# Kernel tuning notes

Measured on AMD Instinct MI355X. Metric: run time of the kernel, lower is better.

The kernel has to match this reference:

```python
import jax, jax.numpy as jnp
import numpy as np

B, T, D_IN = 64, 256, 256
H, N, W, R, D_OUT = 512, 128, 64, 4, 256
CTRL_IN = D_IN + R * W          # 512
IFACE = R * W + R + W + 1 + W + W + R * 3  # 465
EPS = 1e-8


def setup_inputs() -> dict:
    key = jax.random.key(0)
    ks = jax.random.split(key, 10)
    def lin(k, out_d, in_d):
        s = 1.0 / np.sqrt(in_d)
        return jax.random.uniform(k, (out_d, in_d), jnp.float32, -s, s)
    def vec(k, d, in_d):
        s = 1.0 / np.sqrt(in_d)
        return jax.random.uniform(k, (d,), jnp.float32, -s, s)
    return {
        'x': jax.random.normal(ks[0], (B, T, D_IN), jnp.float32),
        'W_ih': lin(ks[1], 4 * H, CTRL_IN),
        'W_hh': lin(ks[2], 4 * H, H),
        'b_ih': vec(ks[3], 4 * H, H),
        'b_hh': vec(ks[4], 4 * H, H),
        'W_int': lin(ks[5], IFACE, H),
        'b_int': vec(ks[6], IFACE, H),
        'W_out': lin(ks[7], D_OUT, H + R * W),
        'b_out': vec(ks[8], D_OUT, H + R * W),
    }


def _content_weights(mem, keys, strength):
    # mem: (b, n, w); keys: (b, r, w); strength: (b, r, 1) -> weights (b, r, n)
    dot = jnp.einsum('brw,bnw->brn', keys, mem)
    nm = jnp.maximum(jnp.linalg.norm(mem, axis=-1), EPS)      # (b, n)
    nk = jnp.maximum(jnp.linalg.norm(keys, axis=-1), EPS)     # (b, r)
    sim = dot / (nk[:, :, None] * nm[:, None, :])
    return jax.nn.softmax(strength * sim, axis=-1)


def reference(x, W_ih, W_hh, b_ih, b_hh, W_int, b_int, W_out, b_out):
    b = x.shape[0]

    def step(carry, x_t):
        h, c, mem, rv = carry
        ci = jnp.concatenate([x_t, rv.reshape(b, R * W)], axis=-1)
        gates = ci @ W_ih.T + b_ih + h @ W_hh.T + b_hh
        i_g, f_g, g_g, o_g = jnp.split(gates, 4, axis=-1)  # torch LSTM gate order
        c = jax.nn.sigmoid(f_g) * c + jax.nn.sigmoid(i_g) * jnp.tanh(g_g)
        h = jax.nn.sigmoid(o_g) * jnp.tanh(c)

        iface = h @ W_int.T + b_int
        idx = 0
        read_keys = iface[:, idx:idx + R * W].reshape(b, R, W); idx += R * W
        read_str = jax.nn.softplus(iface[:, idx:idx + R]) + 1.0; idx += R
        write_key = iface[:, idx:idx + W]; idx += W
        write_str = jax.nn.softplus(iface[:, idx:idx + 1]) + 1.0; idx += 1
        erase = jax.nn.sigmoid(iface[:, idx:idx + W]); idx += W
        write_vec = iface[:, idx:idx + W]; idx += W
        # read_modes are parsed in the original but never used -> skipped

        ww = _content_weights(mem, write_key[:, None, :], write_str[:, None, :])[:, 0, :]  # (b, n)
        mem = mem * (1.0 - ww[:, :, None] * erase[:, None, :]) + ww[:, :, None] * write_vec[:, None, :]

        rw = _content_weights(mem, read_keys, read_str[:, :, None])  # (b, r, n)
        rv = jnp.einsum('brn,bnw->brw', rw, mem)

        out = jnp.concatenate([h, rv.reshape(b, R * W)], axis=-1) @ W_out.T + b_out
        return (h, c, mem, rv), out

    init = (jnp.zeros((b, H), x.dtype), jnp.zeros((b, H), x.dtype),
            jnp.zeros((b, N, W), x.dtype), jnp.zeros((b, R, W), x.dtype))
    _, outs = jax.lax.scan(step, init, jnp.swapaxes(x, 0, 1))  # outs: (T, b, D_OUT)
    return outs[-1]  # return_sequence=False -> last timestep
```

## Files before the change

### kernel.cpp

```cpp
#include <hip/hip_runtime.h>
#include <math.h>

#define BB_   64
#define TT_   256
#define DIN_  256
#define HH_   512
#define NMEM_ 128
#define WWID_ 64
#define RR_   4
#define DOUT_ 256
#define CTRL_ 512
#define EPSV  1e-8f
#define NBLK  256
#define NTHR  512
#define OSTR  456
#define MPAD  65

__device__ __forceinline__ float sigm(float x){ return 1.f/(1.f+expf(-x)); }
__device__ __forceinline__ float softp(float x){ return (x>20.f)? x : log1pf(expf(x)); }
__device__ __forceinline__ float wredsum(float v){
  #pragma unroll
  for (int o=32;o>0;o>>=1) v += __shfl_xor(v,o,64);
  return v;
}
__device__ __forceinline__ float wredmax(float v){
  #pragma unroll
  for (int o=32;o>0;o>>=1) v = fmaxf(v, __shfl_xor(v,o,64));
  return v;
}

__device__ __forceinline__ float2 cload2(const float* p){
  unsigned long long u = __hip_atomic_load((const unsigned long long*)p,
                          __ATOMIC_RELAXED, __HIP_MEMORY_SCOPE_AGENT);
  float2 r; __builtin_memcpy(&r, &u, 8); return r;
}
__device__ __forceinline__ void cstore2(float* p, float2 v){
  unsigned long long u; __builtin_memcpy(&u, &v, 8);
  __hip_atomic_store((unsigned long long*)p, u, __ATOMIC_RELAXED,
                     __HIP_MEMORY_SCOPE_AGENT);
}
__device__ __forceinline__ void cstore1(float* p, float v){
  unsigned u; __builtin_memcpy(&u, &v, 4);
  __hip_atomic_store((unsigned*)p, u, __ATOMIC_RELAXED, __HIP_MEMORY_SCOPE_AGENT);
}
__device__ __forceinline__ unsigned cloadu(const unsigned* p){
  return __hip_atomic_load(p, __ATOMIC_RELAXED, __HIP_MEMORY_SCOPE_AGENT);
}
__device__ __forceinline__ void cincr(unsigned* p){
  __hip_atomic_fetch_add(p, 1u, __ATOMIC_RELAXED, __HIP_MEMORY_SCOPE_AGENT);
}

__global__ void k_initbar(unsigned* bar){
  int i = blockIdx.x*256 + threadIdx.x;
  if (i < 576)
    __hip_atomic_store(bar + i, 0u, __ATOMIC_RELAXED, __HIP_MEMORY_SCOPE_AGENT);
}

__global__ void k_prep_w(const float* __restrict__ Wint, float* __restrict__ WiT4){
  const int o  = blockIdx.x;
  const int kq = threadIdx.x;
  float4 v = *(const float4*)(Wint + (size_t)o*HH_ + 4*kq);
  *(float4*)(WiT4 + ((size_t)kq*OSTR + o)*4) = v;
}

struct Params {
  const float *x, *Wih, *Whh, *bih, *bhh, *bint, *Wout, *bout;
  float *out;
  float *hp;
  float *rvp;
  float *WiT4;
  unsigned *bar;
};

union __align__(16) SMu {
  struct {
    float4 actS[2048];
    float  red[4][4][16][8];
  } a;
  float redO[4][4][64];
  struct {
    float hS[HH_];
    float ifcS[OSTR];
    float kpk[WWID_][8];
    float dH[4][NMEM_];
    float qH[4][NMEM_];
    float nH[4][NMEM_];
    float drH[4][RR_][NMEM_];
    float wwS[NMEM_];
    float rwS[RR_][NMEM_];
    float rvH[8][64];
    float scal[8];
    float red2[8];
  } c;
};

__launch_bounds__(NTHR, 2)
__global__ void k_persist(Params p)
{
  __shared__ SMu sm;
  __shared__ float memS[NMEM_][MPAD];

  const int bi  = blockIdx.x;
  const int tid = threadIdx.x;
  const int b   = tid & 63;
  const int wv  = tid >> 6;
  const int rg  = bi & 31;
  const int col = bi >> 5;
  const int j0  = rg*16;
  const int B0  = col*8;
  const bool isBC = (rg < 8);
  const int bb  = col*8 + rg;

  unsigned* colA = p.bar + col*32;
  unsigned* colC = p.bar + 256 + col*32;

  const int ksA = tid >> 7;
  const int jlA = (tid >> 3) & 15;
  const int blA = tid & 7;

  float c_reg = 0.f;

  const float* wbg[4];
  {
    const float* wsrc = (ksA < 2) ? p.Wih : p.Whh;
    const int koff = (ksA & 1) * 256;
    #pragma unroll
    for (int g = 0; g < 4; ++g)
      wbg[g] = wsrc + (size_t)(g*HH_ + j0 + jlA)*CTRL_ + koff;
  }

  float bsum[4];
  if (tid < 128) {
    const int j = j0 + (tid >> 3);
    #pragma unroll
    for (int g = 0; g < 4; ++g)
      bsum[g] = p.bih[g*HH_ + j] + p.bhh[g*HH_ + j];
  }
  float bintR = 0.f;
  if (isBC && tid < 453) bintR = p.bint[tid];

  {
    const float2 zz = make_float2(0.f, 0.f);
    const int gt = bi*NTHR + tid;
    if      (gt < 16384) cstore2(p.hp  + 2*gt,         zz);
    else if (gt < 24576) cstore2(p.rvp + 2*(gt-16384), zz);
    if (isBC)
      for (int i = tid; i < NMEM_*MPAD; i += NTHR)
        ((float*)memS)[i] = 0.f;
  }
  __syncthreads();
  if (tid == 0) {
    cincr(p.bar + 512);
    while (cloadu(p.bar + 512) < (unsigned)NBLK) __builtin_amdgcn_s_sleep(2);
  }
  __syncthreads();

  for (int t = 0; t < TT_; ++t) {
    const int cur = t & 1, nxt = cur ^ 1;
    const float* hR = p.hp + cur*32768;
    float*       hW = p.hp + nxt*32768;

    if (t > 0) {
      if (tid == 0)
        while (cloadu(colC) < 8u*(unsigned)t) __builtin_amdgcn_s_sleep(1);
      __syncthreads();
    }

    {
      #pragma unroll
      for (int i = 0; i < 4; ++i) {
        const int idx = tid + 512*i;
        const int kq = idx >> 3, bl = idx & 7, bg = B0 + bl;
        float4 v;
        if (kq < 64) {
          v = *(const float4*)(p.x + (size_t)bg*(TT_*DIN_)
                               + (size_t)t*DIN_ + kq*4);
        } else if (kq < 128) {
          const float* s = p.rvp + (kq-64)*256 + bg*4;
          float2 lo = cload2(s), hi = cload2(s + 2);
          v = make_float4(lo.x, lo.y, hi.x, hi.y);
        } else {
          const float* s = hR + (kq-128)*256 + bg*4;
          float2 lo = cload2(s), hi = cload2(s + 2);
          v = make_float4(lo.x, lo.y, hi.x, hi.y);
        }
        sm.a.actS[idx] = v;
      }
      __syncthreads();

      float4 ac[4];
      #pragma unroll
      for (int g = 0; g < 4; ++g) ac[g] = make_float4(0.f, 0.f, 0.f, 0.f);

      const int kbase = ksA*64;
      #pragma unroll 4
      for (int i = 0; i < 64; ++i) {
        float4 a = sm.a.actS[(kbase + i)*8 + blA];
        #pragma unroll
        for (int g = 0; g < 4; ++g) {
          float4 w = *(const float4*)(wbg[g] + (i << 2));
          ac[g].x += w.x*a.x; ac[g].y += w.y*a.y;
          ac[g].z += w.z*a.z; ac[g].w += w.w*a.w;
        }
      }
      #pragma unroll
      for (int g = 0; g < 4; ++g)
        sm.a.red[ksA][g][jlA][blA] = (ac[g].x + ac[g].y) + (ac[g].z + ac[g].w);
      __syncthreads();

      if (tid < 128) {
        const int jl = tid >> 3, bl = tid & 7;
        float gs[4];
        #pragma unroll
        for (int g = 0; g < 4; ++g)
          gs[g] = sm.a.red[0][g][jl][bl] + sm.a.red[1][g][jl][bl]
                + sm.a.red[2][g][jl][bl] + sm.a.red[3][g][jl][bl] + bsum[g];
        float cn = sigm(gs[1])*c_reg + sigm(gs[0])*tanhf(gs[2]);
        c_reg = cn;
        float hn = sigm(gs[3])*tanhf(cn);
        const int j = j0 + jl, bg = B0 + bl;
        cstore1(hW + (j>>2)*256 + bg*4 + (j&3), hn);
      }
    }
    __syncthreads();
    if (tid == 0) cincr(colA);

    if (isBC) {
      if (tid == 0)
        while (cloadu(colA) < 32u*(unsigned)(t+1)) __builtin_amdgcn_s_sleep(1);
      __syncthreads();

      if (tid < 128) {
        const float* hsrc = hW + tid*256 + bb*4;
        float2 lo = cload2(hsrc), hi = cload2(hsrc + 2);
        sm.c.hS[4*tid]   = lo.x; sm.c.hS[4*tid+1] = lo.y;
        sm.c.hS[4*tid+2] = hi.x; sm.c.hS[4*tid+3] = hi.y;
      }
      __syncthreads();
      {
        const int o = (tid < 453) ? tid : 452;
        float a0 = bintR, a1 = 0.f, a2 = 0.f, a3 = 0.f;
        #pragma unroll 8
        for (int kq = 0; kq < 128; ++kq) {
          float4 w  = *(const float4*)(p.WiT4 + ((size_t)kq*OSTR + o)*4);
          float4 h4 = *(const float4*)&sm.c.hS[kq << 2];
          a0 += w.x*h4.x; a1 += w.y*h4.y; a2 += w.z*h4.z; a3 += w.w*h4.w;
        }
        if (tid < 453) sm.c.ifcS[tid] = (a0 + a1) + (a2 + a3);
      }
      __syncthreads();

      if (tid < 64) {
        const int w = tid;
        float wk = sm.c.ifcS[260+w];
        float q0 = sm.c.ifcS[w],      q1 = sm.c.ifcS[64+w];
        float q2 = sm.c.ifcS[128+w],  q3 = sm.c.ifcS[192+w];
        float er  = sigm(sm.c.ifcS[325+w]);
        float wvc = sm.c.ifcS[389+w];
        sm.c.kpk[w][0]=wk; sm.c.kpk[w][1]=q0; sm.c.kpk[w][2]=q1; sm.c.kpk[w][3]=q2;
        sm.c.kpk[w][4]=q3; sm.c.kpk[w][5]=er; sm.c.kpk[w][6]=wvc; sm.c.kpk[w][7]=0.f;
        float s0 = wredsum(wk*wk);
        float s1 = wredsum(q0*q0);
        float s2 = wredsum(q1*q1);
        float s3 = wredsum(q2*q2);
        float s4 = wredsum(q3*q3);
        if (w == 0) {
          sm.c.scal[0] = fmaxf(sqrtf(s0), EPSV);
          sm.c.scal[1] = fmaxf(sqrtf(s1), EPSV);
          sm.c.scal[2] = fmaxf(sqrtf(s2), EPSV);
          sm.c.scal[3] = fmaxf(sqrtf(s3), EPSV);
          sm.c.scal[4] = fmaxf(sqrtf(s4), EPSV);
        }
      }
      __syncthreads();

      const int n  = tid & 127;
      const int wh = tid >> 7;

      {
        float dotw = 0.f, q = 0.f;
        const int w0 = wh*16;
        #pragma unroll
        for (int w = 0; w < 16; ++w) {
          float m = memS[n][w0+w];
          dotw += sm.c.kpk[w0+w][0]*m;
          q    += m*m;
        }
        sm.c.dH[wh][n] = dotw;
        sm.c.qH[wh][n] = q;
      }
      __syncthreads();

      float a_n = 0.f, e_n = 0.f;
      const float wstr = softp(sm.c.ifcS[324]) + 1.f;
      if (tid < 128) {
        float dot = sm.c.dH[0][n] + sm.c.dH[1][n] + sm.c.dH[2][n] + sm.c.dH[3][n];
        float q2  = sm.c.qH[0][n] + sm.c.qH[1][n] + sm.c.qH[2][n] + sm.c.qH[3][n];
        a_n = wstr * dot / (sm.c.scal[0] * fmaxf(sqrtf(q2), EPSV));
        float mx = wredmax(a_n);
        if ((tid & 63) == 0) sm.c.red2[tid>>6] = mx;
      }
      __syncthreads();
      if (tid < 128) {
        float mx = fmaxf(sm.c.red2[0], sm.c.red2[1]);
        e_n = expf(a_n - mx);
        float s = wredsum(e_n);
        if ((tid & 63) == 0) sm.c.red2[4 + (tid>>6)] = s;
      }
      __syncthreads();
      if (tid < 128)
        sm.c.wwS[n] = e_n / (sm.c.red2[4] + sm.c.red2[5]);
      __syncthreads();

      {
        float ww_n = sm.c.wwS[n];
        float nrm=0.f, d0=0.f, d1=0.f, d2=0.f, d3=0.f;
        const int w0 = wh*16;
        #pragma unroll
        for (int w = 0; w < 16; ++w) {
          float4 k0 = *(const float4*)&sm.c.kpk[w0+w][0];
          float4 k1 = *(const float4*)&sm.c.kpk[w0+w][4];
          float m  = memS[n][w0+w];
          float mn = m*(1.f - ww_n*k1.y) + ww_n*k1.z;
          memS[n][w0+w] = mn;
          nrm += mn*mn;
          d0 += k0.y*mn; d1 += k0.z*mn; d2 += k0.w*mn; d3 += k1.x*mn;
        }
        sm.c.nH[wh][n] = nrm;
        sm.c.drH[wh][0][n]=d0; sm.c.drH[wh][1][n]=d1;
        sm.c.drH[wh][2][n]=d2; sm.c.drH[wh][3][n]=d3;
      }
      __syncthreads();

      if (tid < 128) {
        float nrm = sm.c.nH[0][n] + sm.c.nH[1][n] + sm.c.nH[2][n] + sm.c.nH[3][n];
        float inm = 1.f / fmaxf(sqrtf(nrm), EPSV);
        #pragma unroll
        for (int r = 0; r < RR_; ++r) {
          float rstr = softp(sm.c.ifcS[256+r]) + 1.f;
          float dr = sm.c.drH[0][r][n] + sm.c.drH[1][r][n]
                   + sm.c.drH[2][r][n] + sm.c.drH[3][r][n];
          sm.c.rwS[r][n] = rstr * dr * inm / sm.c.scal[1+r];
        }
      }
      __syncthreads();

      if (tid < 256) {
        float v0 = sm.c.rwS[wv][b], v1 = sm.c.rwS[wv][b+64];
        float mx = wredmax(fmaxf(v0, v1));
        float e0 = expf(v0-mx), e1 = expf(v1-mx);
        float s  = wredsum(e0+e1);
        sm.c.rwS[wv][b]    = e0/s;
        sm.c.rwS[wv][b+64] = e1/s;
      }
      __syncthreads();

      {
        const int r  = wv >> 1;
        const int n0 = (wv & 1) * 64;
        float acc = 0.f;
        #pragma unroll 4
        for (int n2 = n0; n2 < n0 + 64; n2 += 4) {
          float4 r4 = *(const float4*)&sm.c.rwS[r][n2];
          acc += r4.x*memS[n2][b]   + r4.y*memS[n2+1][b]
               + r4.z*memS[n2+2][b] + r4.w*memS[n2+3][b];
        }
        sm.c.rvH[wv][b] = acc;
      }
      __syncthreads();
      if (tid < 256) {
        const int r = tid >> 6;
        float acc = sm.c.rvH[2*r][b] + sm.c.rvH[2*r+1][b];
        const int k = r*64 + b;
        cstore1(p.rvp + (k>>2)*256 + bb*4 + (k&3), acc);
      }
      __syncthreads();
      if (tid == 0) cincr(colC);
    }
  }

  if (bi < 64) {
    if (tid == 0) {
      #pragma unroll
      for (int c2 = 0; c2 < 8; ++c2)
        while (cloadu(p.bar + 256 + c2*32) < 8u*(unsigned)TT_)
          __builtin_amdgcn_s_sleep(1);
    }
    __syncthreads();
    const int o0 = bi*4;
    if (tid < 256) {
      float acc[4] = {0.f, 0.f, 0.f, 0.f};
      #pragma unroll 4
      for (int kk = 0; kk < 48; ++kk) {
        const int k = wv*192 + kk*4;
        const float* a8 = (k < 512)
          ? (p.hp  + (((k    )>>2)*64 + b)*4)
          : (p.rvp + (((k-512)>>2)*64 + b)*4);
        float2 alo = cload2(a8);
        float2 ahi = cload2(a8 + 2);
        #pragma unroll
        for (int r = 0; r < 4; ++r) {
          float4 w = *(const float4*)(p.Wout + (size_t)(o0+r)*(HH_ + RR_*WWID_) + k);
          acc[r] += w.x*alo.x + w.y*alo.y + w.z*ahi.x + w.w*ahi.y;
        }
      }
      #pragma unroll
      for (int r = 0; r < 4; ++r) sm.redO[wv][r][b] = acc[r];
    }
    __syncthreads();
    if (tid < 64) {
      float4 o4;
      float* po = (float*)&o4;
      #pragma unroll
      for (int r = 0; r < 4; ++r)
        po[r] = sm.redO[0][r][b] + sm.redO[1][r][b] + sm.redO[2][r][b]
              + sm.redO[3][r][b] + p.bout[o0+r];
      *(float4*)(p.out + (size_t)b*DOUT_ + o0) = o4;
    }
  }
}

extern "C" void kernel_launch(void* const* d_in, const int* in_sizes, int n_in,
                              void* d_out, int out_size, void* d_ws, size_t ws_size,
                              hipStream_t stream)
{
  Params prm;
  prm.x    = (const float*)d_in[0];
  prm.Wih  = (const float*)d_in[1];
  prm.Whh  = (const float*)d_in[2];
  prm.bih  = (const float*)d_in[3];
  prm.bhh  = (const float*)d_in[4];
  const float* Wint = (const float*)d_in[5];
  prm.bint = (const float*)d_in[6];
  prm.Wout = (const float*)d_in[7];
  prm.bout = (const float*)d_in[8];
  prm.out  = (float*)d_out;

  float* ws = (float*)d_ws;
  size_t off = 0;
  prm.hp   = ws + off; off += 2*32768;
  prm.rvp  = ws + off; off += 16384;
  prm.WiT4 = ws + off; off += (size_t)128*OSTR*4;
  prm.bar  = (unsigned*)(ws + off); off += 1024;

  k_prep_w<<<453, 128, 0, stream>>>(Wint, prm.WiT4);
  k_initbar<<<3, 256, 0, stream>>>(prm.bar);
  k_persist<<<NBLK, NTHR, 0, stream>>>(prm);
}
```

Measured before the change: 8.318 ms.

## Split persistent kernel into dedicated LSTM and memory-head blocks with overlapped x-projection

The 256 uniform blocks, where some also ran the memory head, become 128 LSTM-gate blocks (32 hidden units each) plus 64 dedicated per-batch memory/interface blocks. LSTM blocks compute the x and h contributions before waiting for the read-vector barrier, then add only the rv part afterward. This takes the rv-independent work off the critical path between timesteps and removes the serialized gate+memory work from the same block. The cost is fewer total blocks and changed barrier counts, which could cause imbalance or deadlock if block residency is insufficient.

```diff
diff --git a/kernel.cpp b/kernel.cpp
--- a/kernel.cpp
+++ b/kernel.cpp
@@ -11,7 +11,8 @@
 #define DOUT_ 256
 #define CTRL_ 512
 #define EPSV  1e-8f
-#define NBLK  256
+#define NBLK  192
+#define NA_   128
 #define NTHR  512
 #define OSTR  456
 #define MPAD  65
@@ -74,8 +75,8 @@
 
 union __align__(16) SMu {
   struct {
-    float4 actS[2048];
-    float  red[4][4][16][8];
+    float4 actS[1536];
+    float  red[2][4][32][8];
   } a;
   float redO[4][4][64];
   struct {
@@ -104,47 +105,46 @@
   const int tid = threadIdx.x;
   const int b   = tid & 63;
   const int wv  = tid >> 6;
-  const int rg  = bi & 31;
-  const int col = bi >> 5;
-  const int j0  = rg*16;
+  const bool isA = (bi < NA_);
+  const int col = isA ? (bi >> 4) : ((bi - NA_) >> 3);
+  const int rg  = bi & 15;
+  const int j0  = rg*32;
   const int B0  = col*8;
-  const bool isBC = (rg < 8);
-  const int bb  = col*8 + rg;
+  const int bb  = bi - NA_;
 
   unsigned* colA = p.bar + col*32;
   unsigned* colC = p.bar + 256 + col*32;
 
-  const int ksA = tid >> 7;
-  const int jlA = (tid >> 3) & 15;
   const int blA = tid & 7;
+  const int jlA = (tid >> 3) & 31;
+  const int ksA = tid >> 8;
 
   float c_reg = 0.f;
 
   const float* wbg[4];
-  {
-    const float* wsrc = (ksA < 2) ? p.Wih : p.Whh;
-    const int koff = (ksA & 1) * 256;
+  if (isA) {
+    const float* wsrc = (ksA == 0) ? p.Wih : p.Whh;
     #pragma unroll
     for (int g = 0; g < 4; ++g)
-      wbg[g] = wsrc + (size_t)(g*HH_ + j0 + jlA)*CTRL_ + koff;
+      wbg[g] = wsrc + (size_t)(g*HH_ + j0 + jlA)*CTRL_;
   }
 
   float bsum[4];
-  if (tid < 128) {
+  if (isA && tid < 256) {
     const int j = j0 + (tid >> 3);
     #pragma unroll
     for (int g = 0; g < 4; ++g)
       bsum[g] = p.bih[g*HH_ + j] + p.bhh[g*HH_ + j];
   }
   float bintR = 0.f;
-  if (isBC && tid < 453) bintR = p.bint[tid];
+  if (!isA && tid < 453) bintR = p.bint[tid];
 
   {
     const float2 zz = make_float2(0.f, 0.f);
     const int gt = bi*NTHR + tid;
     if      (gt < 16384) cstore2(p.hp  + 2*gt,         zz);
     else if (gt < 24576) cstore2(p.rvp + 2*(gt-16384), zz);
-    if (isBC)
+    if (!isA)
       for (int i = tid; i < NMEM_*MPAD; i += NTHR)
         ((float*)memS)[i] = 0.f;
   }
@@ -155,231 +155,264 @@
   }
   __syncthreads();
 
-  for (int t = 0; t < TT_; ++t) {
-    const int cur = t & 1, nxt = cur ^ 1;
-    const float* hR = p.hp + cur*32768;
-    float*       hW = p.hp + nxt*32768;
-
-    if (t > 0) {
+  if (isA) {
+    for (int t = 0; t < TT_; ++t) {
+      const int cur = t & 1, nxt = cur ^ 1;
+      const float* hR = p.hp + cur*32768;
+      float*       hW = p.hp + nxt*32768;
+
+      if (t > 0) {
+        if (tid == 0)
+          while (cloadu(colA) < 16u*(unsigned)t) __builtin_amdgcn_s_sleep(1);
+        __syncthreads();
+      }
+
+      #pragma unroll
+      for (int i = 0; i < 2; ++i) {
+        const int idx = tid + 512*i;
+        const int kq = idx >> 3, bl = idx & 7;
+        const float* s = hR + kq*256 + (B0 + bl)*4;
+        float2 lo = cload2(s), hi = cload2(s + 2);
+        sm.a.actS[512 + idx] = make_float4(lo.x, lo.y, hi.x, hi.y);
+      }
+      __syncthreads();
+
+      float4 ac[4];
+      #pragma unroll
+      for (int g = 0; g < 4; ++g) ac[g] = make_float4(0.f, 0.f, 0.f, 0.f);
+
+      if (ksA == 0) {
+        const float* xp = p.x + (size_t)(B0 + blA)*(TT_*DIN_) + (size_t)t*DIN_;
+        #pragma unroll 4
+        for (int i = 0; i < 64; ++i) {
+          float4 a = *(const float4*)(xp + 4*i);
+          #pragma unroll
+          for (int g = 0; g < 4; ++g) {
+            float4 w = *(const float4*)(wbg[g] + 4*i);
+            ac[g].x += w.x*a.x; ac[g].y += w.y*a.y;
+            ac[g].z += w.z*a.z; ac[g].w += w.w*a.w;
+          }
+        }
+      } else {
+        #pragma unroll 4
+        for (int i = 0; i < 128; ++i) {
+          float4 a = sm.a.actS[512 + i*8 + blA];
+          #pragma unroll
+          for (int g = 0; g < 4; ++g) {
+            float4 w = *(const float4*)(wbg[g] + 4*i);
+            ac[g].x += w.x*a.x; ac[g].y += w.y*a.y;
+            ac[g].z += w.z*a.z; ac[g].w += w.w*a.w;
+          }
+        }
+        #pragma unroll
+        for (int g = 0; g < 4; ++g)
+          sm.a.red[1][g][jlA][blA] = (ac[g].x + ac[g].y) + (ac[g].z + ac[g].w);
+      }
+
       if (tid == 0)
         while (cloadu(colC) < 8u*(unsigned)t) __builtin_amdgcn_s_sleep(1);
       __syncthreads();
-    }
-
-    {
-      #pragma unroll
-      for (int i = 0; i < 4; ++i) {
-        const int idx = tid + 512*i;
-        const int kq = idx >> 3, bl = idx & 7, bg = B0 + bl;
-        float4 v;
-        if (kq < 64) {
-          v = *(const float4*)(p.x + (size_t)bg*(TT_*DIN_)
-                               + (size_t)t*DIN_ + kq*4);
-        } else if (kq < 128) {
-          const float* s = p.rvp + (kq-64)*256 + bg*4;
-          float2 lo = cload2(s), hi = cload2(s + 2);
-          v = make_float4(lo.x, lo.y, hi.x, hi.y);
-        } else {
-          const float* s = hR + (kq-128)*256 + bg*4;
-          float2 lo = cload2(s), hi = cload2(s + 2);
-          v = make_float4(lo.x, lo.y, hi.x, hi.y);
+
+      {
+        const int kq = tid >> 3, bl = tid & 7;
+        const float* s = p.rvp + kq*256 + (B0 + bl)*4;
+        float2 lo = cload2(s), hi = cload2(s + 2);
+        sm.a.actS[tid] = make_float4(lo.x, lo.y, hi.x, hi.y);
+      }
+      __syncthreads();
+
+      if (ksA == 0) {
+        #pragma unroll 4
+        for (int i = 0; i < 64; ++i) {
+          float4 a = sm.a.actS[i*8 + blA];
+          #pragma unroll
+          for (int g = 0; g < 4; ++g) {
+            float4 w = *(const float4*)(wbg[g] + 4*(64 + i));
+            ac[g].x += w.x*a.x; ac[g].y += w.y*a.y;
+            ac[g].z += w.z*a.z; ac[g].w += w.w*a.w;
+          }
         }
-        sm.a.actS[idx] = v;
+        #pragma unroll
+        for (int g = 0; g < 4; ++g)
+          sm.a.red[0][g][jlA][blA] = (ac[g].x + ac[g].y) + (ac[g].z + ac[g].w);
       }
       __syncthreads();
 
-      float4 ac[4];
-      #pragma unroll
-      for (int g = 0; g < 4; ++g) ac[g] = make_float4(0.f, 0.f, 0.f, 0.f);
-
-      const int kbase = ksA*64;
-      #pragma unroll 4
-      for (int i = 0; i < 64; ++i) {
-        float4 a = sm.a.actS[(kbase + i)*8 + blA];
-        #pragma unroll
-        for (int g = 0; g < 4; ++g) {
-          float4 w = *(const float4*)(wbg[g] + (i << 2));
-          ac[g].x += w.x*a.x; ac[g].y += w.y*a.y;
-          ac[g].z += w.z*a.z; ac[g].w += w.w*a.w;
-        }
-      }
-      #pragma unroll
-      for (int g = 0; g < 4; ++g)
-        sm.a.red[ksA][g][jlA][blA] = (ac[g].x + ac[g].y) + (ac[g].z + ac[g].w);
-      __syncthreads();
-
-      if (tid < 128) {
+      if (tid < 256) {
         const int jl = tid >> 3, bl = tid & 7;
         float gs[4];
         #pragma unroll
         for (int g = 0; g < 4; ++g)
-          gs[g] = sm.a.red[0][g][jl][bl] + sm.a.red[1][g][jl][bl]
-                + sm.a.red[2][g][jl][bl] + sm.a.red[3][g][jl][bl] + bsum[g];
+          gs[g] = sm.a.red[0][g][jl][bl] + sm.a.red[1][g][jl][bl] + bsum[g];
         float cn = sigm(gs[1])*c_reg + sigm(gs[0])*tanhf(gs[2]);
         c_reg = cn;
         float hn = sigm(gs[3])*tanhf(cn);
         const int j = j0 + jl, bg = B0 + bl;
         cstore1(hW + (j>>2)*256 + bg*4 + (j&3), hn);
       }
-    }
-    __syncthreads();
-    if (tid == 0) cincr(colA);
-
-    if (isBC) {
-      if (tid == 0)
-        while (cloadu(colA) < 32u*(unsigned)(t+1)) __builtin_amdgcn_s_sleep(1);
       __syncthreads();
-
-      if (tid < 128) {
-        const float* hsrc = hW + tid*256 + bb*4;
-        float2 lo = cload2(hsrc), hi = cload2(hsrc + 2);
-        sm.c.hS[4*tid]   = lo.x; sm.c.hS[4*tid+1] = lo.y;
-        sm.c.hS[4*tid+2] = hi.x; sm.c.hS[4*tid+3] = hi.y;
-      }
-      __syncthreads();
-      {
-        const int o = (tid < 453) ? tid : 452;
-        float a0 = bintR, a1 = 0.f, a2 = 0.f, a3 = 0.f;
-        #pragma unroll 8
-        for (int kq = 0; kq < 128; ++kq) {
-          float4 w  = *(const float4*)(p.WiT4 + ((size_t)kq*OSTR + o)*4);
-          float4 h4 = *(const float4*)&sm.c.hS[kq << 2];
-          a0 += w.x*h4.x; a1 += w.y*h4.y; a2 += w.z*h4.z; a3 += w.w*h4.w;
-        }
-        if (tid < 453) sm.c.ifcS[tid] = (a0 + a1) + (a2 + a3);
-      }
-      __syncthreads();
-
-      if (tid < 64) {
-        const int w = tid;
-        float wk = sm.c.ifcS[260+w];
-        float q0 = sm.c.ifcS[w],      q1 = sm.c.ifcS[64+w];
-        float q2 = sm.c.ifcS[128+w],  q3 = sm.c.ifcS[192+w];
-        float er  = sigm(sm.c.ifcS[325+w]);
-        float wvc = sm.c.ifcS[389+w];
-        sm.c.kpk[w][0]=wk; sm.c.kpk[w][1]=q0; sm.c.kpk[w][2]=q1; sm.c.kpk[w][3]=q2;
-        sm.c.kpk[w][4]=q3; sm.c.kpk[w][5]=er; sm.c.kpk[w][6]=wvc; sm.c.kpk[w][7]=0.f;
-        float s0 = wredsum(wk*wk);
-        float s1 = wredsum(q0*q0);
-        float s2 = wredsum(q1*q1);
-        float s3 = wredsum(q2*q2);
-        float s4 = wredsum(q3*q3);
-        if (w == 0) {
-          sm.c.scal[0] = fmaxf(sqrtf(s0), EPSV);
-          sm.c.scal[1] = fmaxf(sqrtf(s1), EPSV);
-          sm.c.scal[2] = fmaxf(sqrtf(s2), EPSV);
-          sm.c.scal[3] = fmaxf(sqrtf(s3), EPSV);
-          sm.c.scal[4] = fmaxf(sqrtf(s4), EPSV);
-        }
-      }
-      __syncthreads();
-
-      const int n  = tid & 127;
-      const int wh = tid >> 7;
-
-      {
-        float dotw = 0.f, q = 0.f;
-        const int w0 = wh*16;
-        #pragma unroll
-        for (int w = 0; w < 16; ++w) {
-          float m = memS[n][w0+w];
-          dotw += sm.c.kpk[w0+w][0]*m;
-          q    += m*m;
-        }
-        sm.c.dH[wh][n] = dotw;
-        sm.c.qH[wh][n] = q;
-      }
-      __syncthreads();
-
-      float a_n = 0.f, e_n = 0.f;
-      const float wstr = softp(sm.c.ifcS[324]) + 1.f;
-      if (tid < 128) {
-        float dot = sm.c.dH[0][n] + sm.c.dH[1][n] + sm.c.dH[2][n] + sm.c.dH[3][n];
-        float q2  = sm.c.qH[0][n] + sm.c.qH[1][n] + sm.c.qH[2][n] + sm.c.qH[3][n];
-        a_n = wstr * dot / (sm.c.scal[0] * fmaxf(sqrtf(q2), EPSV));
-        float mx = wredmax(a_n);
-        if ((tid & 63) == 0) sm.c.red2[tid>>6] = mx;
-      }
-      __syncthreads();
-      if (tid < 128) {
-        float mx = fmaxf(sm.c.red2[0], sm.c.red2[1]);
-        e_n = expf(a_n - mx);
-        float s = wredsum(e_n);
-        if ((tid & 63) == 0) sm.c.red2[4 + (tid>>6)] = s;
-      }
-      __syncthreads();
-      if (tid < 128)
-        sm.c.wwS[n] = e_n / (sm.c.red2[4] + sm.c.red2[5]);
-      __syncthreads();
-
-      {
-        float ww_n = sm.c.wwS[n];
-        float nrm=0.f, d0=0.f, d1=0.f, d2=0.f, d3=0.f;
-        const int w0 = wh*16;
-        #pragma unroll
-        for (int w = 0; w < 16; ++w) {
-          float4 k0 = *(const float4*)&sm.c.kpk[w0+w][0];
-          float4 k1 = *(const float4*)&sm.c.kpk[w0+w][4];
-          float m  = memS[n][w0+w];
-          float mn = m*(1.f - ww_n*k1.y) + ww_n*k1.z;
-          memS[n][w0+w] = mn;
-          nrm += mn*mn;
-          d0 += k0.y*mn; d1 += k0.z*mn; d2 += k0.w*mn; d3 += k1.x*mn;
-        }
-        sm.c.nH[wh][n] = nrm;
-        sm.c.drH[wh][0][n]=d0; sm.c.drH[wh][1][n]=d1;
-        sm.c.drH[wh][2][n]=d2; sm.c.drH[wh][3][n]=d3;
-      }
-      __syncthreads();
-
-      if (tid < 128) {
-        float nrm = sm.c.nH[0][n] + sm.c.nH[1][n] + sm.c.nH[2][n] + sm.c.nH[3][n];
-        float inm = 1.f / fmaxf(sqrtf(nrm), EPSV);
-        #pragma unroll
-        for (int r = 0; r < RR_; ++r) {
-          float rstr = softp(sm.c.ifcS[256+r]) + 1.f;
-          float dr = sm.c.drH[0][r][n] + sm.c.drH[1][r][n]
-                   + sm.c.drH[2][r][n] + sm.c.drH[3][r][n];
-          sm.c.rwS[r][n] = rstr * dr * inm / sm.c.scal[1+r];
-        }
-      }
-      __syncthreads();
-
-      if (tid < 256) {
-        float v0 = sm.c.rwS[wv][b], v1 = sm.c.rwS[wv][b+64];
-        float mx = wredmax(fmaxf(v0, v1));
-        float e0 = expf(v0-mx), e1 = expf(v1-mx);
-        float s  = wredsum(e0+e1);
-        sm.c.rwS[wv][b]    = e0/s;
-        sm.c.rwS[wv][b+64] = e1/s;
-      }
-      __syncthreads();
-
-      {
-        const int r  = wv >> 1;
-        const int n0 = (wv & 1) * 64;
-        float acc = 0.f;
-        #pragma unroll 4
-        for (int n2 = n0; n2 < n0 + 64; n2 += 4) {
-          float4 r4 = *(const float4*)&sm.c.rwS[r][n2];
-          acc += r4.x*memS[n2][b]   + r4.y*memS[n2+1][b]
-               + r4.z*memS[n2+2][b] + r4.w*memS[n2+3][b];
-        }
-        sm.c.rvH[wv][b] = acc;
-      }
-      __syncthreads();
-      if (tid < 256) {
-        const int r = tid >> 6;
-        float acc = sm.c.rvH[2*r][b] + sm.c.rvH[2*r+1][b];
-        const int k = r*64 + b;
-        cstore1(p.rvp + (k>>2)*256 + bb*4 + (k&3), acc);
-      }
-      __syncthreads();
-      if (tid == 0) cincr(colC);
-    }
-  }
-
-  if (bi < 64) {
+      if (tid == 0) cincr(colA);
+    }
+    return;
+  }
+
+  for (int t = 0; t < TT_; ++t) {
+    const int nxt = (t & 1) ^ 1;
+    float* hW = p.hp + nxt*32768;
+
+    if (tid == 0)
+      while (cloadu(colA) < 16u*(unsigned)(t+1)) __builtin_amdgcn_s_sleep(1);
+    __syncthreads();
+
+    if (tid < 128) {
+      const float* hsrc = hW + tid*256 + bb*4;
+      float2 lo = cload2(hsrc), hi = cload2(hsrc + 2);
+      sm.c.hS[4*tid]   = lo.x; sm.c.hS[4*tid+1] = lo.y;
+      sm.c.hS[4*tid+2] = hi.x; sm.c.hS[4*tid+3] = hi.y;
+    }
+    __syncthreads();
+    {
+      const int o = (tid < 453) ? tid : 452;
+      float a0 = bintR, a1 = 0.f, a2 = 0.f, a3 = 0.f;
+      #pragma unroll 8
+      for (int kq = 0; kq < 128; ++kq) {
+        float4 w  = *(const float4*)(p.WiT4 + ((size_t)kq*OSTR + o)*4);
+        float4 h4 = *(const float4*)&sm.c.hS[kq << 2];
+        a0 += w.x*h4.x; a1 += w.y*h4.y; a2 += w.z*h4.z; a3 += w.w*h4.w;
+      }
+      if (tid < 453) sm.c.ifcS[tid] = (a0 + a1) + (a2 + a3);
+    }
+    __syncthreads();
+
+    if (tid < 64) {
+      const int w = tid;
+      float wk = sm.c.ifcS[260+w];
+      float q0 = sm.c.ifcS[w],      q1 = sm.c.ifcS[64+w];
+      float q2 = sm.c.ifcS[128+w],  q3 = sm.c.ifcS[192+w];
+      float er  = sigm(sm.c.ifcS[325+w]);
+      float wvc = sm.c.ifcS[389+w];
+      sm.c.kpk[w][0]=wk; sm.c.kpk[w][1]=q0; sm.c.kpk[w][2]=q1; sm.c.kpk[w][3]=q2;
+      sm.c.kpk[w][4]=q3; sm.c.kpk[w][5]=er; sm.c.kpk[w][6]=wvc; sm.c.kpk[w][7]=0.f;
+      float s0 = wredsum(wk*wk);
+      float s1 = wredsum(q0*q0);
+      float s2 = wredsum(q1*q1);
+      float s3 = wredsum(q2*q2);
+      float s4 = wredsum(q3*q3);
+      if (w == 0) {
+        sm.c.scal[0] = fmaxf(sqrtf(s0), EPSV);
+        sm.c.scal[1] = fmaxf(sqrtf(s1), EPSV);
+        sm.c.scal[2] = fmaxf(sqrtf(s2), EPSV);
+        sm.c.scal[3] = fmaxf(sqrtf(s3), EPSV);
+        sm.c.scal[4] = fmaxf(sqrtf(s4), EPSV);
+      }
+    }
+    __syncthreads();
+
+    const int n  = tid & 127;
+    const int wh = tid >> 7;
+
+    {
+      float dotw = 0.f, q = 0.f;
+      const int w0 = wh*16;
+      #pragma unroll
+      for (int w = 0; w < 16; ++w) {
+        float m = memS[n][w0+w];
+        dotw += sm.c.kpk[w0+w][0]*m;
+        q    += m*m;
+      }
+      sm.c.dH[wh][n] = dotw;
+      sm.c.qH[wh][n] = q;
+    }
+    __syncthreads();
+
+    float a_n = 0.f, e_n = 0.f;
+    const float wstr = softp(sm.c.ifcS[324]) + 1.f;
+    if (tid < 128) {
+      float dot = sm.c.dH[0][n] + sm.c.dH[1][n] + sm.c.dH[2][n] + sm.c.dH[3][n];
+      float q2  = sm.c.qH[0][n] + sm.c.qH[1][n] + sm.c.qH[2][n] + sm.c.qH[3][n];
+      a_n = wstr * dot / (sm.c.scal[0] * fmaxf(sqrtf(q2), EPSV));
+      float mx = wredmax(a_n);
+      if ((tid & 63) == 0) sm.c.red2[tid>>6] = mx;
+    }
+    __syncthreads();
+    if (tid < 128) {
+      float mx = fmaxf(sm.c.red2[0], sm.c.red2[1]);
+      e_n = expf(a_n - mx);
+      float s = wredsum(e_n);
+      if ((tid & 63) == 0) sm.c.red2[4 + (tid>>6)] = s;
+    }
+    __syncthreads();
+    if (tid < 128)
+      sm.c.wwS[n] = e_n / (sm.c.red2[4] + sm.c.red2[5]);
+    __syncthreads();
+
+    {
+      float ww_n = sm.c.wwS[n];
+      float nrm=0.f, d0=0.f, d1=0.f, d2=0.f, d3=0.f;
+      const int w0 = wh*16;
+      #pragma unroll
+      for (int w = 0; w < 16; ++w) {
+        float4 k0 = *(const float4*)&sm.c.kpk[w0+w][0];
+        float4 k1 = *(const float4*)&sm.c.kpk[w0+w][4];
+        float m  = memS[n][w0+w];
+        float mn = m*(1.f - ww_n*k1.y) + ww_n*k1.z;
+        memS[n][w0+w] = mn;
+        nrm += mn*mn;
+        d0 += k0.y*mn; d1 += k0.z*mn; d2 += k0.w*mn; d3 += k1.x*mn;
+      }
+      sm.c.nH[wh][n] = nrm;
+      sm.c.drH[wh][0][n]=d0; sm.c.drH[wh][1][n]=d1;
+      sm.c.drH[wh][2][n]=d2; sm.c.drH[wh][3][n]=d3;
+    }
+    __syncthreads();
+
+    if (tid < 128) {
+      float nrm = sm.c.nH[0][n] + sm.c.nH[1][n] + sm.c.nH[2][n] + sm.c.nH[3][n];
+      float inm = 1.f / fmaxf(sqrtf(nrm), EPSV);
+      #pragma unroll
+      for (int r = 0; r < RR_; ++r) {
+        float rstr = softp(sm.c.ifcS[256+r]) + 1.f;
+        float dr = sm.c.drH[0][r][n] + sm.c.drH[1][r][n]
+                 + sm.c.drH[2][r][n] + sm.c.drH[3][r][n];
+        sm.c.rwS[r][n] = rstr * dr * inm / sm.c.scal[1+r];
+      }
+    }
+    __syncthreads();
+
+    if (tid < 256) {
+      float v0 = sm.c.rwS[wv][b], v1 = sm.c.rwS[wv][b+64];
+      float mx = wredmax(fmaxf(v0, v1));
+      float e0 = expf(v0-mx), e1 = expf(v1-mx);
+      float s  = wredsum(e0+e1);
+      sm.c.rwS[wv][b]    = e0/s;
+      sm.c.rwS[wv][b+64] = e1/s;
+    }
+    __syncthreads();
+
+    {
+      const int r  = wv >> 1;
+      const int n0 = (wv & 1) * 64;
+      float acc = 0.f;
+      #pragma unroll 4
+      for (int n2 = n0; n2 < n0 + 64; n2 += 4) {
+        float4 r4 = *(const float4*)&sm.c.rwS[r][n2];
+        acc += r4.x*memS[n2][b]   + r4.y*memS[n2+1][b]
+             + r4.z*memS[n2+2][b] + r4.w*memS[n2+3][b];
+      }
+      sm.c.rvH[wv][b] = acc;
+    }
+    __syncthreads();
+    if (tid < 256) {
+      const int r = tid >> 6;
+      float acc = sm.c.rvH[2*r][b] + sm.c.rvH[2*r+1][b];
+      const int k = r*64 + b;
+      cstore1(p.rvp + (k>>2)*256 + bb*4 + (k&3), acc);
+    }
+    __syncthreads();
+    if (tid == 0) cincr(colC);
+  }
+
+  {
     if (tid == 0) {
       #pragma unroll
       for (int c2 = 0; c2 < 8; ++c2)
@@ -387,7 +420,7 @@
           __builtin_amdgcn_s_sleep(1);
     }
     __syncthreads();
-    const int o0 = bi*4;
+    const int o0 = bb*4;
     if (tid < 256) {
       float acc[4] = {0.f, 0.f, 0.f, 0.f};
       #pragma unroll 4
```

Measured after the change: 13.65 ms. 1.64x slower.
